# Performance work log

Measured on AMD Instinct MI355X. Metric: run time of the kernel, lower is better.

## Reference

```python
import jax, jax.numpy as jnp
import numpy as np

L, NB, B, S, D = 4, 8, 16, 512, 512   # layers, blocks/pathway, batch, seq, dim
K = 2            # max_active_blocks (top-k routing)
FUSION = 0.3     # fusion_strength
PRIOR = 0.5      # fresh block priority: 0.5*0.6 + 0.5*0.4
EPS = 1e-5


def setup_inputs() -> dict:
    key = jax.random.key(0)
    ks = jax.random.split(key, 16)
    rn = lambda k, shp, s=0.02: jax.random.normal(k, shp, dtype=jnp.float32) * s
    return {
        'cortical_input': rn(ks[0], (B, S, D), 1.0),
        'brainstem_input': rn(ks[1], (B, S, D), 1.0),
        'torsion_field': rn(ks[2], (1, D), 1.0),
        'w_sel_c': rn(ks[3], (L, D, NB)), 'b_sel_c': jnp.zeros((L, NB), jnp.float32),
        'w_sel_b': rn(ks[4], (L, D, NB)), 'b_sel_b': jnp.zeros((L, NB), jnp.float32),
        'c_ln_g': jnp.ones((L, NB, D), jnp.float32), 'c_ln_b': jnp.zeros((L, NB, D), jnp.float32),
        'c_w1': rn(ks[5], (L, NB, D, 2 * D)), 'c_b1': jnp.zeros((L, NB, 2 * D), jnp.float32),
        'c_w2': rn(ks[6], (L, NB, 2 * D, D)), 'c_b2': jnp.zeros((L, NB, D), jnp.float32),
        'c_gate': rn(ks[7], (L, NB, D), 0.01),
        'b_ln_g': jnp.ones((L, NB, D), jnp.float32), 'b_ln_b': jnp.zeros((L, NB, D), jnp.float32),
        'b_w1': rn(ks[8], (L, NB, D, D)), 'b_b1': jnp.zeros((L, NB, D), jnp.float32),
        'b_w2': rn(ks[9], (L, NB, D, D)), 'b_b2': jnp.zeros((L, NB, D), jnp.float32),
        'b_gate': rn(ks[10], (L, NB, D), 0.01),
        'w_cross': rn(ks[11], (L, 2 * D, D)), 'b_cross': jnp.zeros((L, D), jnp.float32),
    }


def _block(x, torsion, signal, g, beta, w1, b1, w2, b2, gate, act):
    # LayerNorm -> MLP -> torsion gate -> cross-pathway fusion -> residual*0.5
    mu = x.mean(-1, keepdims=True)
    var = ((x - mu) ** 2).mean(-1, keepdims=True)
    h = (x - mu) * jax.lax.rsqrt(var + EPS) * g + beta
    h = act(h @ w1 + b1) @ w2 + b2
    tg = jax.nn.sigmoid(gate)                 # [D]
    h = h * (1.0 + (tg * torsion)[:, None, :])  # torsion_field: [1,D] -> [1,1,D]
    h = h + signal * tg                        # pathway_signal [B,1,D] * fusion_weight [D]
    return x + 0.5 * h


def _pathway(x, other, torsion, wsel, bsel, g, beta, w1, b1, w2, b2, gate, act):
    scores = jax.nn.sigmoid(x.mean(1) @ wsel + bsel)     # [B, NB]
    adjusted = scores[0] * 0.7 + PRIOR * 0.3             # routing uses sample 0
    _, top = jax.lax.top_k(adjusted, K)
    signal = other.mean(1, keepdims=True) * FUSION       # [B,1,D]
    h = x
    for j in range(K):  # sequential application of the K selected blocks
        i = top[j]
        h = _block(h, torsion, signal, g[i], beta[i], w1[i], b1[i], w2[i], b2[i], gate[i], act)
    return h


def _forward(cortical_input, brainstem_input, torsion_field,
             w_sel_c, b_sel_c, w_sel_b, b_sel_b,
             c_ln_g, c_ln_b, c_w1, c_b1, c_w2, c_b2, c_gate,
             b_ln_g, b_ln_b, b_w1, b_b1, b_w2, b_b2, b_gate,
             w_cross, b_cross):
    c, b = cortical_input, brainstem_input
    gelu = lambda v: jax.nn.gelu(v, approximate=False)
    fused = None
    for l in range(L):
        c_in, b_in = c, b
        c = _pathway(c_in, b_in, torsion_field, w_sel_c[l], b_sel_c[l],
                     c_ln_g[l], c_ln_b[l], c_w1[l], c_b1[l], c_w2[l], c_b2[l], c_gate[l], gelu)
        b = _pathway(b_in, c_in, torsion_field, w_sel_b[l], b_sel_b[l],
                     b_ln_g[l], b_ln_b[l], b_w1[l], b_b1[l], b_w2[l], b_b2[l], b_gate[l], jnp.tanh)
        fused = jnp.concatenate([c, b], axis=-1) @ w_cross[l] + b_cross[l]
    return c, b, fused


def reference(cortical_input, brainstem_input, torsion_field,
              w_sel_c, b_sel_c, w_sel_b, b_sel_b,
              c_ln_g, c_ln_b, c_w1, c_b1, c_w2, c_b2, c_gate,
              b_ln_g, b_ln_b, b_w1, b_b1, b_w2, b_b2, b_gate,
              w_cross, b_cross):
    return _forward(cortical_input, brainstem_input, torsion_field,
                    w_sel_c, b_sel_c, w_sel_b, b_sel_b,
                    c_ln_g, c_ln_b, c_w1, c_b1, c_w2, c_b2, c_gate,
                    b_ln_g, b_ln_b, b_w1, b_b1, b_w2, b_b2, b_gate,
                    w_cross, b_cross)
```

## Files before the change

### kernel.cpp

```cpp
#include <hip/hip_runtime.h>
#include <hip/hip_bf16.h>
#include <math.h>

typedef short s16x8 __attribute__((ext_vector_type(8)));
typedef float f32x4 __attribute__((ext_vector_type(4)));
typedef unsigned short u16;

#define NB_ 8

__device__ __forceinline__ float bf2f(__hip_bfloat16 v){ return __bfloat162float(v); }
__device__ __forceinline__ __hip_bfloat16 f2bf(float v){ return __float2bfloat16(v); }
__device__ __forceinline__ u16 f2u(float v){ __hip_bfloat16 b = f2bf(v); return *(u16*)&b; }

__device__ __forceinline__ float fsigm(float x){ return 1.0f / (1.0f + __expf(-x)); }
__device__ __forceinline__ float ftanh(float x){ return 1.0f - 2.0f / (__expf(2.0f * x) + 1.0f); }
__device__ __forceinline__ float fgelu(float x){
    return 0.5f * x * (1.0f + ftanh(0.79788456080286536f * (x + 0.044715f * x * x * x)));
}

__device__ __forceinline__ void async16(u16* lds, const u16* g)
{
    __builtin_amdgcn_global_load_lds((const __attribute__((address_space(1))) void*)g,
                                     (__attribute__((address_space(3))) void*)lds,
                                     16, 0, 0);
}

struct GArg {
    const u16* A0; const u16* A1; int lda; int ksplit;
    const u16* BT; const float* bias; int bias_stride;
    const float* gate; int gate_stride; const float* meansig;
    u16* outb; float* xio; int N; int K; int idx_off; int mode;
};

__global__ __launch_bounds__(256, 4)
void gemm_dual(GArg ga, GArg gb, int ysplit,
               const int* __restrict__ idxbuf, const float* __restrict__ torsion)
{
    __shared__ __align__(16) u16 sm[4][128 * 32];
    const bool second = (int)blockIdx.y >= ysplit;
    const GArg& g = second ? gb : ga;
    const int n0 = (second ? blockIdx.y - ysplit : blockIdx.y) * 128;
    const int m0 = blockIdx.x * 128;
    const int tid = threadIdx.x;
    const int wave = tid >> 6, lane = tid & 63;
    const int wm = (wave >> 1) * 64, wn = (wave & 1) * 64;
    const int lrow = lane & 15, quad = lane >> 4;

    int rS[2], cS[2];
#pragma unroll
    for (int it = 0; it < 2; it++) {
        int s = wave * 1024 + it * 512 + lane * 8;
        rS[it] = s >> 5;
        cS[it] = s & 31;
    }

    f32x4 acc[4][4] = {};
    const int K = g.K, ksplit = g.ksplit, lda = g.lda, N = g.N;
    const u16* BTn = g.BT + (size_t)n0 * K;
    const int niter = K >> 5;

    auto stage = [&](int k0, int buf) {
        const u16* Ab; int kk;
        if (k0 < ksplit) { Ab = g.A0; kk = k0; }
        else             { Ab = g.A1; kk = k0 - ksplit; }
        const u16* Arow = Ab + (size_t)m0 * lda + kk;
        u16* Ad = &sm[buf][wave * 1024];
        u16* Bd = &sm[2 + buf][wave * 1024];
#pragma unroll
        for (int it = 0; it < 2; it++)
            async16(Ad + it * 512, Arow + (size_t)rS[it] * lda + cS[it]);
#pragma unroll
        for (int it = 0; it < 2; it++)
            async16(Bd + it * 512, BTn + (size_t)rS[it] * K + k0 + cS[it]);
    };

    stage(0, 0);
    __syncthreads();

    for (int k = 0; k < niter; k++) {
        int cur = k & 1, nxt = cur ^ 1;
        if (k + 1 < niter) stage((k + 1) << 5, nxt);
        s16x8 af[4], bfv[4];
#pragma unroll
        for (int i = 0; i < 4; i++)
            af[i] = *(const s16x8*)&sm[cur][(wm + i * 16 + lrow) * 32 + quad * 8];
#pragma unroll
        for (int j = 0; j < 4; j++)
            bfv[j] = *(const s16x8*)&sm[2 + cur][(wn + j * 16 + lrow) * 32 + quad * 8];
#pragma unroll
        for (int i = 0; i < 4; i++)
#pragma unroll
            for (int j = 0; j < 4; j++)
                acc[i][j] = __builtin_amdgcn_mfma_f32_16x16x32_bf16(af[i], bfv[j], acc[i][j], 0, 0, 0);
        __syncthreads();
    }

    const int idx = (g.idx_off >= 0) ? idxbuf[g.idx_off] : 0;
    const float* bias = g.bias + (size_t)idx * g.bias_stride;
    const float* gate = g.gate ? (g.gate + (size_t)idx * g.gate_stride) : nullptr;
    const float* msrow = g.meansig ? (g.meansig + (size_t)(m0 >> 9) * 512) : nullptr;
    const int mode = g.mode;

    if (mode <= 1) {
        u16* CT = &sm[0][0];
#pragma unroll
        for (int j = 0; j < 4; j++) {
            const int n_loc = wn + j * 16 + lrow;
            const float bn = bias[n0 + n_loc];
#pragma unroll
            for (int i = 0; i < 4; i++) {
#pragma unroll
                for (int r = 0; r < 4; r++) {
                    const int m_loc = wm + i * 16 + quad * 4 + r;
                    float v = acc[i][j][r] + bn;
                    v = (mode == 0) ? fgelu(v) : ftanh(v);
                    CT[m_loc * 128 + (n_loc ^ (quad << 4))] = f2u(v);
                }
            }
        }
        __syncthreads();
#pragma unroll
        for (int p = 0; p < 8; p++) {
            int ip  = p * 256 + tid;
            int row = ip >> 4;
            int c0  = (ip & 15) * 8;
            s16x8 vv = *(const s16x8*)&CT[row * 128 + (c0 ^ (((row >> 2) & 3) << 4))];
            *(s16x8*)&g.outb[(size_t)(m0 + row) * N + n0 + c0] = vv;
        }
        return;
    }

#pragma unroll
    for (int j = 0; j < 4; j++) {
        const int n = n0 + wn + j * 16 + lrow;
        const float bn = bias[n];
        float ea = 0.f, ec = 0.f;
        if (mode == 2) {
            float tg  = fsigm(gate[n]);
            float tor = torsion[n];
            ea = 0.5f * (1.0f + tg * tor);
            ec = 0.5f * (msrow[n] * 0.3f) * tg;
        }
#pragma unroll
        for (int i = 0; i < 4; i++) {
#pragma unroll
            for (int r = 0; r < 4; r++) {
                const int m = m0 + wm + i * 16 + quad * 4 + r;
                const size_t off = (size_t)m * N + n;
                float v = acc[i][j][r] + bn;
                if (mode == 2) g.xio[off] = g.xio[off] + ea * v + ec;
                else           g.xio[off] = v;
            }
        }
    }
}

__global__ __launch_bounds__(64)
void ln_dual(const float* __restrict__ xc, const float* __restrict__ xb,
             u16* __restrict__ lnc, u16* __restrict__ lnb,
             const float* __restrict__ cg, const float* __restrict__ cb,
             const float* __restrict__ bg, const float* __restrict__ bb,
             const int* __restrict__ idxbuf, int j)
{
    int bid = blockIdx.x, lane = threadIdx.x;
    bool second = bid >= 8192;
    int row = second ? bid - 8192 : bid;
    const float* x = second ? xb : xc;
    u16* out = second ? lnb : lnc;
    const float* gbase = second ? bg : cg;
    const float* bbase = second ? bb : cb;
    int idx = idxbuf[second ? 2 + j : j];

    const float* xr = x + (size_t)row * 512;
    float4 v0 = *(const float4*)(xr + lane * 8);
    float4 v1 = *(const float4*)(xr + lane * 8 + 4);
    float vals[8] = {v0.x, v0.y, v0.z, v0.w, v1.x, v1.y, v1.z, v1.w};
    float s = 0.f, s2 = 0.f;
#pragma unroll
    for (int t = 0; t < 8; t++) { s += vals[t]; s2 += vals[t] * vals[t]; }
#pragma unroll
    for (int o = 32; o; o >>= 1) { s += __shfl_xor(s, o); s2 += __shfl_xor(s2, o); }
    float mu  = s * (1.f / 512.f);
    float var = s2 * (1.f / 512.f) - mu * mu;
    float rs  = rsqrtf(var + 1e-5f);
    const float* gg  = gbase + (size_t)idx * 512;
    const float* bbp = bbase + (size_t)idx * 512;
    int d0 = lane * 8;
    __align__(16) u16 o8[8];
#pragma unroll
    for (int t = 0; t < 8; t++)
        o8[t] = f2u((vals[t] - mu) * rs * gg[d0 + t] + bbp[d0 + t]);
    *(uint4*)(out + (size_t)row * 512 + d0) = *(const uint4*)o8;
}

__global__ void zero_kernel(float* p, int n)
{
    int i = blockIdx.x * blockDim.x + threadIdx.x;
    if (i < n) p[i] = 0.f;
}

__global__ __launch_bounds__(512)
void mean_kernel(const float* __restrict__ xc, const float* __restrict__ xb,
                 float* __restrict__ mc, float* __restrict__ mb)
{
    int bid = blockIdx.x;
    int half = bid >> 7;
    const float* x = half ? xb : xc;
    float* m = half ? mb : mc;
    int b = (bid & 127) >> 3, ch = bid & 7;
    int d = threadIdx.x;
    const float* p = x + ((size_t)b * 512 + ch * 64) * 512 + d;
    float s = 0.f;
#pragma unroll 8
    for (int i = 0; i < 64; i++) s += p[(size_t)i * 512];
    atomicAdd(&m[b * 512 + d], s * (1.f / 512.f));
}

__global__ __launch_bounds__(128)
void route_kernel(const float* __restrict__ mc, const float* __restrict__ mb,
                  const float* __restrict__ wsel_c, const float* __restrict__ bsel_c,
                  const float* __restrict__ wsel_b, const float* __restrict__ bsel_b,
                  int* __restrict__ idx_out)
{
    int g = threadIdx.x >> 6, lane = threadIdx.x & 63;
    const float* mrow = g ? mb : mc;
    const float* ws = g ? wsel_b : wsel_c;
    const float* bs = g ? bsel_b : bsel_c;
    float acc[8] = {0.f, 0.f, 0.f, 0.f, 0.f, 0.f, 0.f, 0.f};
    for (int d = lane; d < 512; d += 64) {
        float mv = mrow[d];
#pragma unroll
        for (int n = 0; n < 8; n++) acc[n] += mv * ws[d * 8 + n];
    }
#pragma unroll
    for (int o = 32; o; o >>= 1)
#pragma unroll
        for (int n = 0; n < 8; n++) acc[n] += __shfl_xor(acc[n], o);
    if (lane == 0) {
        float adj[8];
#pragma unroll
        for (int n = 0; n < 8; n++) {
            float sc = 1.0f / (1.0f + expf(-(acc[n] + bs[n])));
            adj[n] = 0.7f * sc + 0.15f;
        }
        int i0 = 0;
        for (int n = 1; n < 8; n++) if (adj[n] > adj[i0]) i0 = n;
        int i1 = -1;
        for (int n = 0; n < 8; n++) {
            if (n == i0) continue;
            if (i1 < 0 || adj[n] > adj[i1]) i1 = n;
        }
        idx_out[g * 2 + 0] = i0;
        idx_out[g * 2 + 1] = i1;
    }
}

struct TArg { const float* src; u16* dst; int R; int C; int idx_off; int nblk; };

__global__ __launch_bounds__(256)
void transpose4(TArg t0, TArg t1, TArg t2, TArg t3, const int* __restrict__ idxbuf)
{
    int bid = blockIdx.x;
    TArg t;
    if (bid < t0.nblk) t = t0;
    else { bid -= t0.nblk;
        if (bid < t1.nblk) t = t1;
        else { bid -= t1.nblk;
            if (bid < t2.nblk) t = t2;
            else { bid -= t2.nblk; t = t3; } } }
    int idx = (t.idx_off >= 0) ? idxbuf[t.idx_off] : 0;
    const float* src = t.src + (size_t)idx * t.R * t.C;
    int tpr = t.C >> 5;
    int tr = bid / tpr, tc = bid % tpr;
    __shared__ u16 tile[32][33];
    int tx = threadIdx.x & 31, ty = threadIdx.x >> 5;
#pragma unroll
    for (int r = ty; r < 32; r += 8)
        tile[r][tx] = f2u(src[(size_t)(tr * 32 + r) * t.C + tc * 32 + tx]);
    __syncthreads();
#pragma unroll
    for (int r = ty; r < 32; r += 8)
        t.dst[(size_t)(tc * 32 + r) * t.R + tr * 32 + tx] = tile[tx][r];
}

__global__ __launch_bounds__(256)
void f2b_kernel(const float* __restrict__ xa, const float* __restrict__ xb,
                u16* __restrict__ oa, u16* __restrict__ ob)
{
    int i = (blockIdx.x * 256 + threadIdx.x) * 8;
    const float* src = blockIdx.y ? xb : xa;
    u16* dst = blockIdx.y ? ob : oa;
    float4 f0 = *(const float4*)(src + i);
    float4 f1 = *(const float4*)(src + i + 4);
    float vv[8] = {f0.x, f0.y, f0.z, f0.w, f1.x, f1.y, f1.z, f1.w};
    __align__(16) u16 o8[8];
#pragma unroll
    for (int t = 0; t < 8; t++) o8[t] = f2u(vv[t]);
    *(uint4*)(dst + i) = *(const uint4*)o8;
}

extern "C" void kernel_launch(void* const* d_in, const int* in_sizes, int n_in,
                              void* d_out, int out_size, void* d_ws, size_t ws_size,
                              hipStream_t stream)
{
    const float* in_c   = (const float*)d_in[0];
    const float* in_b   = (const float*)d_in[1];
    const float* torsion= (const float*)d_in[2];
    const float* wsel_c = (const float*)d_in[3];
    const float* bsel_c = (const float*)d_in[4];
    const float* wsel_b = (const float*)d_in[5];
    const float* bsel_b = (const float*)d_in[6];
    const float* c_ln_g = (const float*)d_in[7];
    const float* c_ln_b = (const float*)d_in[8];
    const float* c_w1   = (const float*)d_in[9];
    const float* c_b1   = (const float*)d_in[10];
    const float* c_w2   = (const float*)d_in[11];
    const float* c_b2   = (const float*)d_in[12];
    const float* c_gate = (const float*)d_in[13];
    const float* b_ln_g = (const float*)d_in[14];
    const float* b_ln_b = (const float*)d_in[15];
    const float* b_w1   = (const float*)d_in[16];
    const float* b_b1   = (const float*)d_in[17];
    const float* b_w2   = (const float*)d_in[18];
    const float* b_b2   = (const float*)d_in[19];
    const float* b_gate = (const float*)d_in[20];
    const float* w_cross= (const float*)d_in[21];
    const float* b_cross= (const float*)d_in[22];

    const size_t SD = (size_t)8192 * 512;

    float* x_c  = (float*)d_out;
    float* x_b  = x_c + SD;
    float* out_f = x_b + SD;

    char* w = (char*)d_ws;
    u16* lnc   = (u16*)w; w += SD * 2;
    u16* lnb   = (u16*)w; w += SD * 2;
    u16* act_c = (u16*)w; w += SD * 2 * 2;
    u16* act_b = (u16*)w; w += SD * 2;
    u16* cbf   = (u16*)w; w += SD * 2;
    u16* bbf   = (u16*)w; w += SD * 2;
    float* mean_c = (float*)w; w += (size_t)16 * 512 * 4;
    float* mean_b = (float*)w; w += (size_t)16 * 512 * 4;
    int*   idxbuf = (int*)w;   w += 256;
    u16* w1t_c = (u16*)w; w += (size_t)1024 * 512 * 2;
    u16* w2t_c = (u16*)w; w += (size_t)1024 * 512 * 2;
    u16* w1t_b = (u16*)w; w += (size_t)512 * 512 * 2;
    u16* w2t_b = (u16*)w; w += (size_t)512 * 512 * 2;
    u16* wxT   = (u16*)w; w += (size_t)1024 * 512 * 2;

    hipMemcpyAsync(x_c, in_c, SD * 4, hipMemcpyDeviceToDevice, stream);
    hipMemcpyAsync(x_b, in_b, SD * 4, hipMemcpyDeviceToDevice, stream);

    TArg twx = { w_cross + (size_t)3 * 1024 * 512, wxT, 1024, 512, -1, 512 };
    TArg tz  = { nullptr, nullptr, 32, 32, -1, 0 };
    transpose4<<<512, 256, 0, stream>>>(twx, tz, tz, tz, idxbuf);

    for (int l = 0; l < 4; l++) {
        zero_kernel<<<64, 256, 0, stream>>>(mean_c, 16384);
        mean_kernel<<<256, 512, 0, stream>>>(x_c, x_b, mean_c, mean_b);
        route_kernel<<<1, 128, 0, stream>>>(mean_c, mean_b,
            wsel_c + (size_t)l * 512 * 8, bsel_c + (size_t)l * 8,
            wsel_b + (size_t)l * 512 * 8, bsel_b + (size_t)l * 8, idxbuf);

        for (int j = 0; j < 2; j++) {
            TArg tc1 = { c_w1 + (size_t)l * NB_ * 512 * 1024, w1t_c, 512, 1024, j, 512 };
            TArg tc2 = { c_w2 + (size_t)l * NB_ * 1024 * 512, w2t_c, 1024, 512, j, 512 };
            TArg tb1 = { b_w1 + (size_t)l * NB_ * 512 * 512,  w1t_b, 512, 512, 2 + j, 256 };
            TArg tb2 = { b_w2 + (size_t)l * NB_ * 512 * 512,  w2t_b, 512, 512, 2 + j, 256 };
            transpose4<<<1536, 256, 0, stream>>>(tc1, tc2, tb1, tb2, idxbuf);

            ln_dual<<<16384, 64, 0, stream>>>(x_c, x_b, lnc, lnb,
                c_ln_g + (size_t)l * NB_ * 512, c_ln_b + (size_t)l * NB_ * 512,
                b_ln_g + (size_t)l * NB_ * 512, b_ln_b + (size_t)l * NB_ * 512,
                idxbuf, j);

            GArg g1c = { lnc, nullptr, 512, 1 << 30, w1t_c,
                         c_b1 + (size_t)l * NB_ * 1024, 1024,
                         nullptr, 0, nullptr, act_c, nullptr, 1024, 512, j, 0 };
            GArg g1b = { lnb, nullptr, 512, 1 << 30, w1t_b,
                         b_b1 + (size_t)l * NB_ * 512, 512,
                         nullptr, 0, nullptr, act_b, nullptr, 512, 512, 2 + j, 1 };
            gemm_dual<<<dim3(64, 12), 256, 0, stream>>>(g1c, g1b, 8, idxbuf, torsion);

            GArg g2c = { act_c, nullptr, 1024, 1 << 30, w2t_c,
                         c_b2 + (size_t)l * NB_ * 512, 512,
                         c_gate + (size_t)l * NB_ * 512, 512, mean_b,
                         nullptr, x_c, 512, 1024, j, 2 };
            GArg g2b = { act_b, nullptr, 512, 1 << 30, w2t_b,
                         b_b2 + (size_t)l * NB_ * 512, 512,
                         b_gate + (size_t)l * NB_ * 512, 512, mean_c,
                         nullptr, x_b, 512, 512, 2 + j, 2 };
            gemm_dual<<<dim3(64, 8), 256, 0, stream>>>(g2c, g2b, 4, idxbuf, torsion);
        }
    }

    f2b_kernel<<<dim3(2048, 2), 256, 0, stream>>>(x_c, x_b, cbf, bbf);
    GArg gf = { cbf, bbf, 512, 512, wxT,
                b_cross + (size_t)3 * 512, 0,
                nullptr, 0, nullptr, nullptr, out_f, 512, 1024, -1, 3 };
    gemm_dual<<<dim3(64, 4), 256, 0, stream>>>(gf, gf, 4, idxbuf, torsion);
}
```

Baseline: 954.3 us.

## Triple-buffer GEMM LDS pipeline with XOR swizzle and explicit waitcnt barriers

Moves the GEMM main loop from double to triple buffering in LDS. Tiles are prefetched two iterations ahead, and explicit vmcnt waits and raw barriers replace __syncthreads. An XOR swizzle is applied to the LDS column layout for both the async stores and the fragment reads, to reduce bank conflicts. MFMA issue is wrapped in s_setprio. LDS use rises by half and launch bounds drop to 3 blocks per CU, so occupancy may fall. The epilogue reuses sm[0] and may need to account for the new layout.

```diff
diff --git a/kernel.cpp b/kernel.cpp
--- a/kernel.cpp
+++ b/kernel.cpp
@@ -32,11 +32,11 @@
     u16* outb; float* xio; int N; int K; int idx_off; int mode;
 };
 
-__global__ __launch_bounds__(256, 4)
+__global__ __launch_bounds__(256, 3)
 void gemm_dual(GArg ga, GArg gb, int ysplit,
                const int* __restrict__ idxbuf, const float* __restrict__ torsion)
 {
-    __shared__ __align__(16) u16 sm[4][128 * 32];
+    __shared__ __align__(16) u16 sm[6][128 * 32];
     const bool second = (int)blockIdx.y >= ysplit;
     const GArg& g = second ? gb : ga;
     const int n0 = (second ? blockIdx.y - ysplit : blockIdx.y) * 128;
@@ -45,13 +45,15 @@
     const int wave = tid >> 6, lane = tid & 63;
     const int wm = (wave >> 1) * 64, wn = (wave & 1) * 64;
     const int lrow = lane & 15, quad = lane >> 4;
+    const int coff = ((quad ^ ((lrow >> 1) & 3)) << 3);
 
     int rS[2], cS[2];
 #pragma unroll
     for (int it = 0; it < 2; it++) {
         int s = wave * 1024 + it * 512 + lane * 8;
         rS[it] = s >> 5;
-        cS[it] = s & 31;
+        int p = (s >> 3) & 3;
+        cS[it] = ((p ^ ((rS[it] >> 1) & 3)) << 3);
     }
 
     f32x4 acc[4][4] = {};
@@ -65,7 +67,7 @@
         else             { Ab = g.A1; kk = k0 - ksplit; }
         const u16* Arow = Ab + (size_t)m0 * lda + kk;
         u16* Ad = &sm[buf][wave * 1024];
-        u16* Bd = &sm[2 + buf][wave * 1024];
+        u16* Bd = &sm[3 + buf][wave * 1024];
 #pragma unroll
         for (int it = 0; it < 2; it++)
             async16(Ad + it * 512, Arow + (size_t)rS[it] * lda + cS[it]);
@@ -75,24 +77,46 @@
     };
 
     stage(0, 0);
-    __syncthreads();
-
+    if (niter > 1) stage(32, 1);
+    if (niter > 2) stage(64, 2);
+
+    int cur = 0;
     for (int k = 0; k < niter; k++) {
-        int cur = k & 1, nxt = cur ^ 1;
-        if (k + 1 < niter) stage((k + 1) << 5, nxt);
+        const int left = niter - 1 - k;
+        if (left >= 2)      asm volatile("s_waitcnt vmcnt(8)" ::: "memory");
+        else if (left == 1) asm volatile("s_waitcnt vmcnt(4)" ::: "memory");
+        else                asm volatile("s_waitcnt vmcnt(0)" ::: "memory");
+        __builtin_amdgcn_sched_barrier(0);
+        __builtin_amdgcn_s_barrier();
+        __builtin_amdgcn_sched_barrier(0);
+
+        const u16* Ac = &sm[cur][0];
+        const u16* Bc = &sm[3 + cur][0];
         s16x8 af[4], bfv[4];
 #pragma unroll
         for (int i = 0; i < 4; i++)
-            af[i] = *(const s16x8*)&sm[cur][(wm + i * 16 + lrow) * 32 + quad * 8];
+            af[i] = *(const s16x8*)&Ac[(wm + i * 16 + lrow) * 32 + coff];
 #pragma unroll
         for (int j = 0; j < 4; j++)
-            bfv[j] = *(const s16x8*)&sm[2 + cur][(wn + j * 16 + lrow) * 32 + quad * 8];
+            bfv[j] = *(const s16x8*)&Bc[(wn + j * 16 + lrow) * 32 + coff];
+
+        asm volatile("s_waitcnt lgkmcnt(0)" ::: "memory");
+        __builtin_amdgcn_sched_barrier(0);
+        __builtin_amdgcn_s_barrier();
+        __builtin_amdgcn_sched_barrier(0);
+
+        if (k + 3 < niter) stage((k + 3) << 5, cur);
+
+        __builtin_amdgcn_s_setprio(1);
 #pragma unroll
         for (int i = 0; i < 4; i++)
 #pragma unroll
             for (int j = 0; j < 4; j++)
                 acc[i][j] = __builtin_amdgcn_mfma_f32_16x16x32_bf16(af[i], bfv[j], acc[i][j], 0, 0, 0);
-        __syncthreads();
+        __builtin_amdgcn_s_setprio(0);
+        __builtin_amdgcn_sched_barrier(0);
+
+        cur = (cur == 2) ? 0 : cur + 1;
     }
 
     const int idx = (g.idx_off >= 0) ? idxbuf[g.idx_off] : 0;
```

New measurement: 931.6 us. 1.02x faster.
